# Optimization experiments

Hardware: AMD Instinct MI355X
Metric: run time of the kernel (lower is better)

Reference implementation:

```python
import jax, jax.numpy as jnp
from jax import lax
import numpy as np

DIM = 512
NUM_HEADS = 8
SR = 2


def setup_inputs() -> dict:
    key = jax.random.key(0)
    ks = jax.random.split(key, 7)
    B, H, W = 4, 64, 64
    N = H * W
    C = DIM
    s = 0.02
    return {
        "x": jax.random.normal(ks[0], (B, N, C), dtype=jnp.float32),
        "q_w": jax.random.normal(ks[1], (C, C), dtype=jnp.float32) * s,
        "kv_w": jax.random.normal(ks[2], (2 * C, C), dtype=jnp.float32) * s,
        "sr_w": jax.random.normal(ks[3], (C, C, SR, SR), dtype=jnp.float32) * s,
        "sr_b": jax.random.normal(ks[4], (C,), dtype=jnp.float32) * s,
        "proj_w": jax.random.normal(ks[5], (C, C), dtype=jnp.float32) * s,
        "proj_b": jax.random.normal(ks[6], (C,), dtype=jnp.float32) * s,
        "H": H,
        "W": W,
    }


def reference(x, q_w, kv_w, sr_w, sr_b, proj_w, proj_b, H, W):
    B, N, C = x.shape
    nh = NUM_HEADS
    hd = C // nh
    scale = hd ** -0.5

    # q projection: [B, nh, N, hd]
    q = (x @ q_w.T).reshape(B, N, nh, hd).transpose(0, 2, 1, 3)

    # spatial reduction via strided conv (kernel=stride=SR)
    x_ = x.transpose(0, 2, 1).reshape(B, C, H, W)
    x_ = lax.conv_general_dilated(
        x_, sr_w, window_strides=(SR, SR), padding="VALID",
        dimension_numbers=("NCHW", "OIHW", "NCHW"),
    ) + sr_b[None, :, None, None]
    Nk = (H // SR) * (W // SR)
    x_ = x_.reshape(B, C, Nk).transpose(0, 2, 1)  # [B, Nk, C]

    # kv projection: [2, B, nh, Nk, hd]
    kv = (x_ @ kv_w.T).reshape(B, Nk, 2, nh, hd).transpose(2, 0, 3, 1, 4)
    k, v = kv[0], kv[1]

    attn = jax.nn.softmax(jnp.einsum("bhnd,bhmd->bhnm", q, k) * scale, axis=-1)
    out = jnp.einsum("bhnm,bhmd->bhnd", attn, v)  # [B, nh, N, hd]
    out = out.transpose(0, 2, 1, 3).reshape(B, N, C)
    return out @ proj_w.T + proj_b
```

## Files before the change

### kernel.cpp

```cpp
#include <hip/hip_runtime.h>


typedef __attribute__((ext_vector_type(8)))  short short8;
typedef __attribute__((ext_vector_type(8)))  unsigned short ushort8;
typedef __attribute__((ext_vector_type(4)))  float floatx4;
typedef __attribute__((ext_vector_type(16))) float floatx16;

__device__ inline unsigned short bf16r(float f) {
    union { float f; unsigned u; } v; v.f = f;
    unsigned r = v.u + 0x7fffu + ((v.u >> 16) & 1u);
    return (unsigned short)(r >> 16);
}

__device__ inline unsigned long long pack4ull(float4 v) {
    return (unsigned long long)bf16r(v.x)
         | ((unsigned long long)bf16r(v.y) << 16)
         | ((unsigned long long)bf16r(v.z) << 32)
         | ((unsigned long long)bf16r(v.w) << 48);
}

__device__ inline ushort8 pack8(float4 a, float4 b) {
    ushort8 o;
    o[0] = bf16r(a.x); o[1] = bf16r(a.y); o[2] = bf16r(a.z); o[3] = bf16r(a.w);
    o[4] = bf16r(b.x); o[5] = bf16r(b.y); o[6] = bf16r(b.z); o[7] = bf16r(b.w);
    return o;
}

__device__ inline void gl_lds16(const void* g, void* l) {
    __builtin_amdgcn_global_load_lds(
        (const __attribute__((address_space(1))) unsigned int*)g,
        (__attribute__((address_space(3))) unsigned int*)l, 16, 0, 0);
}

__global__ __launch_bounds__(256)
void prep(const float* __restrict__ x,  const float* __restrict__ qw,
          const float* __restrict__ kvw, const float* __restrict__ srw,
          const float* __restrict__ pw,
          unsigned short* __restrict__ xb,  unsigned short* __restrict__ qwb,
          unsigned short* __restrict__ kvwb, unsigned short* __restrict__ srwb,
          unsigned short* __restrict__ pwb, unsigned short* __restrict__ xrb) {
    const int bid = blockIdx.x;
    if (bid < 2048) {
        const int id = bid * 256 + threadIdx.x;
        const int cq = id & 127, m = id >> 7;
        const int c0 = cq * 4;
        const int b = m >> 10, rem = m & 1023;
        const int oi = rem >> 5, oj = rem & 31;
        const int n00 = oi * 128 + oj * 2;
        const float* bp = x + ((size_t)(b * 4096 + n00)) * 512 + c0;
        const float4 r00 = *(const float4*)bp;
        const float4 r01 = *(const float4*)(bp + 512);
        const float4 r10 = *(const float4*)(bp + 64 * 512);
        const float4 r11 = *(const float4*)(bp + 65 * 512);
        const unsigned long long w00 = pack4ull(r00), w01 = pack4ull(r01),
                                 w10 = pack4ull(r10), w11 = pack4ull(r11);
        unsigned short* xo = xb + ((size_t)(b * 4096 + n00)) * 512 + c0;
        *(unsigned long long*)(xo)            = w00;
        *(unsigned long long*)(xo + 512)      = w01;
        *(unsigned long long*)(xo + 64 * 512) = w10;
        *(unsigned long long*)(xo + 65 * 512) = w11;
        unsigned short* xd = xrb + (size_t)m * 2048 + c0 * 4;
        #pragma unroll
        for (int j = 0; j < 4; ++j) {
            const unsigned long long e =
                  ((w00 >> (16 * j)) & 0xffffull)
                | (((w01 >> (16 * j)) & 0xffffull) << 16)
                | (((w10 >> (16 * j)) & 0xffffull) << 32)
                | (((w11 >> (16 * j)) & 0xffffull) << 48);
            *(unsigned long long*)(xd + j * 4) = e;
        }
    } else {
        const int b2 = bid - 2048;
        const float* src; unsigned short* dst; int off; float sc = 1.f;
        if (b2 < 128)      { src = qw;  dst = qwb;  off = b2 * 256;
                             sc = 0.18033688011112042f;  }
        else if (b2 < 384) { src = kvw; dst = kvwb; off = (b2 - 128) * 256; }
        else if (b2 < 896) { src = srw; dst = srwb; off = (b2 - 384) * 256; }
        else               { src = pw;  dst = pwb;  off = (b2 - 896) * 256; }
        const int idx = off + threadIdx.x;
        float4 a = *(const float4*)(src + (size_t)idx * 8);
        float4 bq = *(const float4*)(src + (size_t)idx * 8 + 4);
        a.x *= sc; a.y *= sc; a.z *= sc; a.w *= sc;
        bq.x *= sc; bq.y *= sc; bq.z *= sc; bq.w *= sc;
        *(ushort8*)(dst + (size_t)idx * 8) = pack8(a, bq);
    }
}

__device__ __forceinline__ void g_stage(
        const unsigned short* __restrict__ A, const unsigned short* __restrict__ B,
        int K, int bm, int bn, int k0, int t,
        unsigned short* AsB, unsigned short* BsB) {
    #pragma unroll
    for (int i = 0; i < 4; ++i) {
        const int c = i * 256 + t;
        const int r = c >> 3, ch = c & 7;
        gl_lds16(A + (size_t)(bm + r) * K + k0 + ((ch ^ (r & 7)) * 8), AsB + c * 8);
    }
    #pragma unroll
    for (int i = 0; i < 2; ++i) {
        const int c = i * 256 + t;
        const int r = c >> 3, ch = c & 7;
        gl_lds16(B + (size_t)(bn + r) * K + k0 + ((ch ^ (r & 7)) * 8), BsB + c * 8);
    }
}

__device__ __forceinline__ void g_comp(
        const unsigned short* AsB, const unsigned short* BsB,
        int lq, int quad, int wrow, floatx4 (&acc)[2][4]) {
    short8 bf[2][4];
    #pragma unroll
    for (int kc = 0; kc < 2; ++kc)
        #pragma unroll
        for (int ni = 0; ni < 4; ++ni) {
            const int r = ni * 16 + lq;
            bf[kc][ni] = *(const short8*)&BsB[r * 64 + (((kc * 4 + quad) ^ (r & 7)) * 8)];
        }
    #pragma unroll
    for (int mi = 0; mi < 2; ++mi) {
        const int r = wrow + mi * 16 + lq;
        #pragma unroll
        for (int kc = 0; kc < 2; ++kc) {
            const short8 af = *(const short8*)&AsB[r * 64 + (((kc * 4 + quad) ^ (r & 7)) * 8)];
            #pragma unroll
            for (int ni = 0; ni < 4; ++ni)
                acc[mi][ni] = __builtin_amdgcn_mfma_f32_16x16x32_bf16(
                    af, bf[kc][ni], acc[mi][ni], 0, 0, 0);
        }
    }
}

__device__ __forceinline__ void g_run(
        const unsigned short* __restrict__ A, const unsigned short* __restrict__ B,
        int K, int bm, int bn, int t, int lq, int quad, int wrow,
        unsigned short (&As)[2][128 * 64], unsigned short (&Bs)[2][64 * 64],
        floatx4 (&acc)[2][4]) {
    g_stage(A, B, K, bm, bn, 0, t, As[0], Bs[0]);
    __syncthreads();
    const int nk = K >> 6;
    for (int ks = 0; ks < nk; ++ks) {
        const int cur = ks & 1;
        if (ks + 1 < nk)
            g_stage(A, B, K, bm, bn, (ks + 1) * 64, t, As[cur ^ 1], Bs[cur ^ 1]);
        __builtin_amdgcn_s_setprio(1);
        g_comp(As[cur], Bs[cur], lq, quad, wrow, acc);
        __builtin_amdgcn_s_setprio(0);
        if (ks + 1 < nk) __syncthreads();
    }
}

__global__ __launch_bounds__(256)
void gemm_qc(const unsigned short* __restrict__ xb, const unsigned short* __restrict__ qwb,
             const unsigned short* __restrict__ xrb, const unsigned short* __restrict__ srwb,
             const float* __restrict__ sr_b,
             unsigned short* __restrict__ qb, unsigned short* __restrict__ xsrb) {
    __shared__ unsigned short As[2][128 * 64];
    __shared__ unsigned short Bs[2][64 * 64];
    const int t = threadIdx.x;
    const int w = t >> 6, l = t & 63;
    const int lq = l & 15, quad = l >> 4;
    const int wrow = w * 32;
    const int bx = blockIdx.x;
    const unsigned short *A, *B; int K, bm; const float* bias; unsigned short* C;
    if (bx < 128) { A = xb;  B = qwb;  K = 512;  bm = bx * 128;         bias = nullptr; C = qb;   }
    else          { A = xrb; B = srwb; K = 2048; bm = (bx - 128) * 128; bias = sr_b;    C = xsrb; }
    const int bn = blockIdx.y * 64;

    floatx4 acc[2][4];
    #pragma unroll
    for (int mi = 0; mi < 2; ++mi)
        #pragma unroll
        for (int ni = 0; ni < 4; ++ni) acc[mi][ni] = (floatx4){0.f, 0.f, 0.f, 0.f};

    g_run(A, B, K, bm, bn, t, lq, quad, wrow, As, Bs, acc);

    #pragma unroll
    for (int ni = 0; ni < 4; ++ni) {
        const int col = bn + ni * 16 + lq;
        const float bv = bias ? bias[col] : 0.f;
        #pragma unroll
        for (int mi = 0; mi < 2; ++mi) {
            const int row0 = bm + wrow + mi * 16 + quad * 4;
            unsigned own[4], mg[4];
            #pragma unroll
            for (int r = 0; r < 4; ++r) own[r] = bf16r(acc[mi][ni][r] + bv);
            #pragma unroll
            for (int r = 0; r < 4; ++r) {
                const unsigned pt = __shfl_xor(own[r], 1);
                mg[r] = (lq & 1) ? (pt | (own[r] << 16)) : (own[r] | (pt << 16));
            }
            const int colb = bn + ni * 16 + (lq & ~1);
            const int rb = (lq & 1) * 2;
            *(unsigned*)(C + (size_t)(row0 + rb)     * 512 + colb) = mg[rb];
            *(unsigned*)(C + (size_t)(row0 + rb + 1) * 512 + colb) = mg[rb + 1];
        }
    }
}

__global__ __launch_bounds__(256)
void gemm_kv(const unsigned short* __restrict__ kvwb, const unsigned short* __restrict__ xsrb,
             unsigned short* __restrict__ Kb, unsigned short* __restrict__ Vt) {
    __shared__ unsigned short As[2][128 * 64];
    __shared__ unsigned short Bs[2][64 * 64];
    const int t = threadIdx.x;
    const int w = t >> 6, l = t & 63;
    const int lq = l & 15, quad = l >> 4;
    const int wrow = w * 32;
    const int id = blockIdx.x;
    const bool isK = id < 256;
    const unsigned short* A = isK ? kvwb : xsrb;
    const unsigned short* B = isK ? xsrb : kvwb + (size_t)512 * 512;
    const int bm = isK ? (id & 3) * 128 : ((id - 256) >> 3) * 128;
    const int bn = isK ? (id >> 2) * 64 : ((id - 256) & 7) * 64;

    floatx4 acc[2][4];
    #pragma unroll
    for (int mi = 0; mi < 2; ++mi)
        #pragma unroll
        for (int ni = 0; ni < 4; ++ni) acc[mi][ni] = (floatx4){0.f, 0.f, 0.f, 0.f};

    g_run(A, B, 512, bm, bn, t, lq, quad, wrow, As, Bs, acc);

    #pragma unroll
    for (int ni = 0; ni < 4; ++ni) {
        const int col = bn + ni * 16 + lq;
        #pragma unroll
        for (int mi = 0; mi < 2; ++mi) {
            const int row0 = bm + wrow + mi * 16 + quad * 4;
            unsigned long long wv = 0;
            #pragma unroll
            for (int r = 0; r < 4; ++r)
                wv |= (unsigned long long)bf16r(acc[mi][ni][r]) << (16 * r);
            if (isK) {
                const int kb = col >> 10, key = col & 1023;
                const int h = row0 >> 6, d0 = row0 & 63;
                *(unsigned long long*)(Kb +
                    (((size_t)(kb * 8 + h)) * 1024 + key) * 64 + d0) = wv;
            } else {
                const int kb = row0 >> 10, key0 = row0 & 1023;
                const int h = col >> 6, d = col & 63;
                *(unsigned long long*)(Vt +
                    (((size_t)(kb * 8 + h)) * 64 + d) * 1024 + key0) = wv;
            }
        }
    }
}

__global__ __launch_bounds__(256)
void gemm_proj(const unsigned short* __restrict__ attb, const unsigned short* __restrict__ pwb,
               const float* __restrict__ pb, float* __restrict__ out) {
    __shared__ unsigned short As[2][128 * 64];
    __shared__ unsigned short Bs[2][64 * 64];
    const int t = threadIdx.x;
    const int w = t >> 6, l = t & 63;
    const int lq = l & 15, quad = l >> 4;
    const int wrow = w * 32;
    const int bm = blockIdx.x * 128, bn = blockIdx.y * 64;

    floatx4 acc[2][4];
    #pragma unroll
    for (int mi = 0; mi < 2; ++mi)
        #pragma unroll
        for (int ni = 0; ni < 4; ++ni) acc[mi][ni] = (floatx4){0.f, 0.f, 0.f, 0.f};

    g_run(attb, pwb, 512, bm, bn, t, lq, quad, wrow, As, Bs, acc);

    #pragma unroll
    for (int ni = 0; ni < 4; ++ni) {
        const int col = bn + ni * 16 + lq;
        const float bv = pb[col];
        #pragma unroll
        for (int mi = 0; mi < 2; ++mi) {
            const int row0 = bm + wrow + mi * 16 + quad * 4;
            #pragma unroll
            for (int r = 0; r < 4; ++r)
                out[(size_t)(row0 + r) * 512 + col] = acc[mi][ni][r] + bv;
        }
    }
}

#define KS2 72

__global__ __launch_bounds__(256)
void attn_mfma32(const unsigned short* __restrict__ qb,
                 const unsigned short* __restrict__ Kb,
                 const unsigned short* __restrict__ Vt,
                 unsigned short* __restrict__ out) {
    __shared__ unsigned short Ks[64 * KS2];
    __shared__ unsigned short Vs[64 * KS2];

    const int t = threadIdx.x;
    const int w = t >> 6;
    const int lane = t & 63;
    const int m32 = lane & 31;
    const int sig = lane >> 5;
    const int n0 = blockIdx.x * 128;
    const int bh = blockIdx.y;
    const int b = bh >> 3, h = bh & 7;

    short8 qf[4];
    {
        const unsigned short* qrow =
            qb + ((size_t)(b * 4096 + n0 + w * 32 + m32)) * 512 + h * 64;
        #pragma unroll
        for (int kc = 0; kc < 4; ++kc)
            qf[kc] = *(const short8*)(qrow + kc * 16 + sig * 8);
    }

    float l_own = 0.f;
    floatx16 O0, O1;
    #pragma unroll
    for (int i = 0; i < 16; ++i) { O0[i] = 0.f; O1[i] = 0.f; }

    const unsigned short* Kg = Kb + (size_t)bh * 1024 * 64;
    const unsigned short* Vg = Vt + (size_t)bh * 64 * 1024;
    const int srow = t >> 2;
    const int sdb  = (t & 3) * 16;

    for (int kt = 0; kt < 16; ++kt) {
        __syncthreads();
        {
            const unsigned short* src = Kg + ((size_t)(kt * 64 + srow)) * 64 + sdb;
            *(ushort8*)&Ks[srow * KS2 + sdb]     = *(const ushort8*)src;
            *(ushort8*)&Ks[srow * KS2 + sdb + 8] = *(const ushort8*)(src + 8);
        }
        {
            const unsigned short* src = Vg + (size_t)srow * 1024 + kt * 64 + sdb;
            *(ushort8*)&Vs[srow * KS2 + sdb]     = *(const ushort8*)src;
            *(ushort8*)&Vs[srow * KS2 + sdb + 8] = *(const ushort8*)(src + 8);
        }
        __syncthreads();

        floatx16 st0, st1;
        #pragma unroll
        for (int i = 0; i < 16; ++i) { st0[i] = 0.f; st1[i] = 0.f; }
        __builtin_amdgcn_s_setprio(1);
        #pragma unroll
        for (int kc = 0; kc < 4; ++kc) {
            const short8 a0 = *(const short8*)&Ks[m32 * KS2 + kc * 16 + sig * 8];
            st0 = __builtin_amdgcn_mfma_f32_32x32x16_bf16(a0, qf[kc], st0, 0, 0, 0);
            const short8 a1 = *(const short8*)&Ks[(32 + m32) * KS2 + kc * 16 + sig * 8];
            st1 = __builtin_amdgcn_mfma_f32_32x32x16_bf16(a1, qf[kc], st1, 0, 0, 0);
        }
        __builtin_amdgcn_s_setprio(0);

        uint2 E[2][4];
        #pragma unroll
        for (int g = 0; g < 2; ++g) {
            #pragma unroll
            for (int qd = 0; qd < 4; ++qd) {
                const float p0 = __builtin_amdgcn_exp2f(g ? st1[qd * 4 + 0] : st0[qd * 4 + 0]);
                const float p1 = __builtin_amdgcn_exp2f(g ? st1[qd * 4 + 1] : st0[qd * 4 + 1]);
                const float p2 = __builtin_amdgcn_exp2f(g ? st1[qd * 4 + 2] : st0[qd * 4 + 2]);
                const float p3 = __builtin_amdgcn_exp2f(g ? st1[qd * 4 + 3] : st0[qd * 4 + 3]);
                E[g][qd].x = __builtin_amdgcn_perm(
                    __float_as_uint(p1), __float_as_uint(p0), 0x07060302u);
                E[g][qd].y = __builtin_amdgcn_perm(
                    __float_as_uint(p3), __float_as_uint(p2), 0x07060302u);
                l_own += (p0 + p1) + (p2 + p3);
            }
        }

        __builtin_amdgcn_s_setprio(1);
        #pragma unroll
        for (int kc = 0; kc < 4; ++kc) {
            const int g = kc >> 1, qlo = (kc & 1) * 2;
            unsigned ax = E[g][qlo].x, bx_ = E[g][qlo + 1].x;
            unsigned ay = E[g][qlo].y, by_ = E[g][qlo + 1].y;
            asm("v_permlane32_swap_b32 %0, %1" : "+v"(ax), "+v"(bx_));
            asm("v_permlane32_swap_b32 %0, %1" : "+v"(ay), "+v"(by_));
            uint4 fr; fr.x = ax; fr.y = ay; fr.z = bx_; fr.w = by_;
            const short8 pa = *(const short8*)&fr;
            const short8 v0 = *(const short8*)&Vs[m32 * KS2 + kc * 16 + sig * 8];
            O0 = __builtin_amdgcn_mfma_f32_32x32x16_bf16(pa, v0, O0, 0, 0, 0);
            const short8 v1 = *(const short8*)&Vs[(32 + m32) * KS2 + kc * 16 + sig * 8];
            O1 = __builtin_amdgcn_mfma_f32_32x32x16_bf16(pa, v1, O1, 0, 0, 0);
        }
        __builtin_amdgcn_s_setprio(0);
    }

    l_own += __shfl_xor(l_own, 32);
    const float inv = 1.0f / l_own;

    float fo0[16], fo1[16];
    #pragma unroll
    for (int r = 0; r < 16; ++r) {
        const float li = __shfl(inv, ((r & 3) + 8 * (r >> 2)) + 4 * sig);
        fo0[r] = O0[r] * li;
        fo1[r] = O1[r] * li;
    }

    #pragma unroll
    for (int gd = 0; gd < 2; ++gd) {
        unsigned mg[16];
        #pragma unroll
        for (int r = 0; r < 16; ++r) {
            const unsigned own = bf16r(gd ? fo1[r] : fo0[r]);
            const unsigned pt = __shfl_xor(own, 1);
            mg[r] = (m32 & 1) ? (pt | (own << 16)) : (own | (pt << 16));
        }
        if ((m32 & 1) == gd) {
            const int colb = h * 64 + gd * 32 + (m32 & ~1);
            #pragma unroll
            for (int r = 0; r < 16; ++r) {
                const int qrow = (r & 3) + 8 * (r >> 2) + 4 * sig;
                const size_t row = (size_t)(b * 4096 + n0 + w * 32 + qrow);
                *(unsigned*)(out + row * 512 + colb) = mg[r];
            }
        }
    }
}

extern "C" void kernel_launch(void* const* d_in, const int* in_sizes, int n_in,
                              void* d_out, int out_size, void* d_ws, size_t ws_size,
                              hipStream_t stream) {
    const float* x      = (const float*)d_in[0];
    const float* q_w    = (const float*)d_in[1];
    const float* kv_w   = (const float*)d_in[2];
    const float* sr_w   = (const float*)d_in[3];
    const float* sr_b   = (const float*)d_in[4];
    const float* proj_w = (const float*)d_in[5];
    const float* proj_b = (const float*)d_in[6];
    float* out = (float*)d_out;

    unsigned short* xb   = (unsigned short*)d_ws;
    unsigned short* attb = xb;
    unsigned short* qb   = xb   + (size_t)16384 * 512;
    unsigned short* xrb  = qb   + (size_t)16384 * 512;
    unsigned short* xsrb = xrb  + (size_t)4096 * 2048;
    unsigned short* qwb  = xsrb + (size_t)4096 * 512;
    unsigned short* kvwb = qwb  + (size_t)512 * 512;
    unsigned short* srwb = kvwb + (size_t)1024 * 512;
    unsigned short* pwb  = srwb + (size_t)512 * 2048;
    unsigned short* Kb   = pwb  + (size_t)512 * 512;
    unsigned short* Vt   = Kb   + (size_t)32 * 1024 * 64;

    const dim3 blk(256);

    prep<<<3072, blk, 0, stream>>>(x, q_w, kv_w, sr_w, proj_w,
                                   xb, qwb, kvwb, srwb, pwb, xrb);

    gemm_qc<<<dim3(160, 8), blk, 0, stream>>>(xb, qwb, xrb, srwb, sr_b, qb, xsrb);

    gemm_kv<<<512, blk, 0, stream>>>(kvwb, xsrb, Kb, Vt);

    attn_mfma32<<<dim3(32, 32), blk, 0, stream>>>(qb, Kb, Vt, attb);

    gemm_proj<<<dim3(128, 8), blk, 0, stream>>>(attb, pwb, proj_b, out);
}
```

Measured before the change: 218.8 us.

## Enlarge GEMM tiles to 128x128 and double attention KV tile with XCD-aware block remap

```diff
diff --git a/kernel.cpp b/kernel.cpp
--- a/kernel.cpp
+++ b/kernel.cpp
@@ -97,7 +97,7 @@
         gl_lds16(A + (size_t)(bm + r) * K + k0 + ((ch ^ (r & 7)) * 8), AsB + c * 8);
     }
     #pragma unroll
-    for (int i = 0; i < 2; ++i) {
+    for (int i = 0; i < 4; ++i) {
         const int c = i * 256 + t;
         const int r = c >> 3, ch = c & 7;
         gl_lds16(B + (size_t)(bn + r) * K + k0 + ((ch ^ (r & 7)) * 8), BsB + c * 8);
@@ -106,34 +106,32 @@
 
 __device__ __forceinline__ void g_comp(
         const unsigned short* AsB, const unsigned short* BsB,
-        int lq, int quad, int wrow, floatx4 (&acc)[2][4]) {
-    short8 bf[2][4];
-    #pragma unroll
-    for (int kc = 0; kc < 2; ++kc)
+        int lq, int quad, int wrow, int wcol, floatx4 (&acc)[4][4]) {
+    #pragma unroll
+    for (int kc = 0; kc < 2; ++kc) {
+        short8 bfq[4];
         #pragma unroll
         for (int ni = 0; ni < 4; ++ni) {
-            const int r = ni * 16 + lq;
-            bf[kc][ni] = *(const short8*)&BsB[r * 64 + (((kc * 4 + quad) ^ (r & 7)) * 8)];
-        }
-    #pragma unroll
-    for (int mi = 0; mi < 2; ++mi) {
-        const int r = wrow + mi * 16 + lq;
-        #pragma unroll
-        for (int kc = 0; kc < 2; ++kc) {
+            const int r = wcol + ni * 16 + lq;
+            bfq[ni] = *(const short8*)&BsB[r * 64 + (((kc * 4 + quad) ^ (r & 7)) * 8)];
+        }
+        #pragma unroll
+        for (int mi = 0; mi < 4; ++mi) {
+            const int r = wrow + mi * 16 + lq;
             const short8 af = *(const short8*)&AsB[r * 64 + (((kc * 4 + quad) ^ (r & 7)) * 8)];
             #pragma unroll
             for (int ni = 0; ni < 4; ++ni)
                 acc[mi][ni] = __builtin_amdgcn_mfma_f32_16x16x32_bf16(
-                    af, bf[kc][ni], acc[mi][ni], 0, 0, 0);
+                    af, bfq[ni], acc[mi][ni], 0, 0, 0);
         }
     }
 }
 
 __device__ __forceinline__ void g_run(
         const unsigned short* __restrict__ A, const unsigned short* __restrict__ B,
-        int K, int bm, int bn, int t, int lq, int quad, int wrow,
-        unsigned short (&As)[2][128 * 64], unsigned short (&Bs)[2][64 * 64],
-        floatx4 (&acc)[2][4]) {
+        int K, int bm, int bn, int t, int lq, int quad, int wrow, int wcol,
+        unsigned short (&As)[2][128 * 64], unsigned short (&Bs)[2][128 * 64],
+        floatx4 (&acc)[4][4]) {
     g_stage(A, B, K, bm, bn, 0, t, As[0], Bs[0]);
     __syncthreads();
     const int nk = K >> 6;
@@ -142,7 +140,7 @@
         if (ks + 1 < nk)
             g_stage(A, B, K, bm, bn, (ks + 1) * 64, t, As[cur ^ 1], Bs[cur ^ 1]);
         __builtin_amdgcn_s_setprio(1);
-        g_comp(As[cur], Bs[cur], lq, quad, wrow, acc);
+        g_comp(As[cur], Bs[cur], lq, quad, wrow, wcol, acc);
         __builtin_amdgcn_s_setprio(0);
         if (ks + 1 < nk) __syncthreads();
     }
@@ -154,31 +152,31 @@
              const float* __restrict__ sr_b,
              unsigned short* __restrict__ qb, unsigned short* __restrict__ xsrb) {
     __shared__ unsigned short As[2][128 * 64];
-    __shared__ unsigned short Bs[2][64 * 64];
+    __shared__ unsigned short Bs[2][128 * 64];
     const int t = threadIdx.x;
     const int w = t >> 6, l = t & 63;
     const int lq = l & 15, quad = l >> 4;
-    const int wrow = w * 32;
+    const int wrow = (w >> 1) * 64, wcol = (w & 1) * 64;
     const int bx = blockIdx.x;
     const unsigned short *A, *B; int K, bm; const float* bias; unsigned short* C;
     if (bx < 128) { A = xb;  B = qwb;  K = 512;  bm = bx * 128;         bias = nullptr; C = qb;   }
     else          { A = xrb; B = srwb; K = 2048; bm = (bx - 128) * 128; bias = sr_b;    C = xsrb; }
-    const int bn = blockIdx.y * 64;
-
-    floatx4 acc[2][4];
-    #pragma unroll
-    for (int mi = 0; mi < 2; ++mi)
+    const int bn = blockIdx.y * 128;
+
+    floatx4 acc[4][4];
+    #pragma unroll
+    for (int mi = 0; mi < 4; ++mi)
         #pragma unroll
         for (int ni = 0; ni < 4; ++ni) acc[mi][ni] = (floatx4){0.f, 0.f, 0.f, 0.f};
 
-    g_run(A, B, K, bm, bn, t, lq, quad, wrow, As, Bs, acc);
+    g_run(A, B, K, bm, bn, t, lq, quad, wrow, wcol, As, Bs, acc);
 
     #pragma unroll
     for (int ni = 0; ni < 4; ++ni) {
-        const int col = bn + ni * 16 + lq;
+        const int col = bn + wcol + ni * 16 + lq;
         const float bv = bias ? bias[col] : 0.f;
         #pragma unroll
-        for (int mi = 0; mi < 2; ++mi) {
+        for (int mi = 0; mi < 4; ++mi) {
             const int row0 = bm + wrow + mi * 16 + quad * 4;
             unsigned own[4], mg[4];
             #pragma unroll
@@ -188,7 +186,7 @@
                 const unsigned pt = __shfl_xor(own[r], 1);
                 mg[r] = (lq & 1) ? (pt | (own[r] << 16)) : (own[r] | (pt << 16));
             }
-            const int colb = bn + ni * 16 + (lq & ~1);
+            const int colb = bn + wcol + ni * 16 + (lq & ~1);
             const int rb = (lq & 1) * 2;
             *(unsigned*)(C + (size_t)(row0 + rb)     * 512 + colb) = mg[rb];
             *(unsigned*)(C + (size_t)(row0 + rb + 1) * 512 + colb) = mg[rb + 1];
@@ -200,31 +198,32 @@
 void gemm_kv(const unsigned short* __restrict__ kvwb, const unsigned short* __restrict__ xsrb,
              unsigned short* __restrict__ Kb, unsigned short* __restrict__ Vt) {
     __shared__ unsigned short As[2][128 * 64];
-    __shared__ unsigned short Bs[2][64 * 64];
+    __shared__ unsigned short Bs[2][128 * 64];
     const int t = threadIdx.x;
     const int w = t >> 6, l = t & 63;
     const int lq = l & 15, quad = l >> 4;
-    const int wrow = w * 32;
+    const int wrow = (w >> 1) * 64, wcol = (w & 1) * 64;
     const int id = blockIdx.x;
-    const bool isK = id < 256;
+    const bool isK = id < 128;
+    const int id2 = isK ? id : id - 128;
     const unsigned short* A = isK ? kvwb : xsrb;
     const unsigned short* B = isK ? xsrb : kvwb + (size_t)512 * 512;
-    const int bm = isK ? (id & 3) * 128 : ((id - 256) >> 3) * 128;
-    const int bn = isK ? (id >> 2) * 64 : ((id - 256) & 7) * 64;
-
-    floatx4 acc[2][4];
-    #pragma unroll
-    for (int mi = 0; mi < 2; ++mi)
+    const int bm = isK ? (id2 & 3) * 128 : (id2 >> 2) * 128;
+    const int bn = isK ? (id2 >> 2) * 128 : (id2 & 3) * 128;
+
+    floatx4 acc[4][4];
+    #pragma unroll
+    for (int mi = 0; mi < 4; ++mi)
         #pragma unroll
         for (int ni = 0; ni < 4; ++ni) acc[mi][ni] = (floatx4){0.f, 0.f, 0.f, 0.f};
 
-    g_run(A, B, 512, bm, bn, t, lq, quad, wrow, As, Bs, acc);
+    g_run(A, B, 512, bm, bn, t, lq, quad, wrow, wcol, As, Bs, acc);
 
     #pragma unroll
     for (int ni = 0; ni < 4; ++ni) {
-        const int col = bn + ni * 16 + lq;
-        #pragma unroll
-        for (int mi = 0; mi < 2; ++mi) {
+        const int col = bn + wcol + ni * 16 + lq;
+        #pragma unroll
+        for (int mi = 0; mi < 4; ++mi) {
             const int row0 = bm + wrow + mi * 16 + quad * 4;
             unsigned long long wv = 0;
             #pragma unroll
@@ -249,27 +248,27 @@
 void gemm_proj(const unsigned short* __restrict__ attb, const unsigned short* __restrict__ pwb,
                const float* __restrict__ pb, float* __restrict__ out) {
     __shared__ unsigned short As[2][128 * 64];
-    __shared__ unsigned short Bs[2][64 * 64];
+    __shared__ unsigned short Bs[2][128 * 64];
     const int t = threadIdx.x;
     const int w = t >> 6, l = t & 63;
     const int lq = l & 15, quad = l >> 4;
-    const int wrow = w * 32;
-    const int bm = blockIdx.x * 128, bn = blockIdx.y * 64;
-
-    floatx4 acc[2][4];
-    #pragma unroll
-    for (int mi = 0; mi < 2; ++mi)
+    const int wrow = (w >> 1) * 64, wcol = (w & 1) * 64;
+    const int bm = blockIdx.x * 128, bn = blockIdx.y * 128;
+
+    floatx4 acc[4][4];
+    #pragma unroll
+    for (int mi = 0; mi < 4; ++mi)
         #pragma unroll
         for (int ni = 0; ni < 4; ++ni) acc[mi][ni] = (floatx4){0.f, 0.f, 0.f, 0.f};
 
-    g_run(attb, pwb, 512, bm, bn, t, lq, quad, wrow, As, Bs, acc);
+    g_run(attb, pwb, 512, bm, bn, t, lq, quad, wrow, wcol, As, Bs, acc);
 
     #pragma unroll
     for (int ni = 0; ni < 4; ++ni) {
-        const int col = bn + ni * 16 + lq;
+        const int col = bn + wcol + ni * 16 + lq;
         const float bv = pb[col];
         #pragma unroll
-        for (int mi = 0; mi < 2; ++mi) {
+        for (int mi = 0; mi < 4; ++mi) {
             const int row0 = bm + wrow + mi * 16 + quad * 4;
             #pragma unroll
             for (int r = 0; r < 4; ++r)
@@ -279,22 +278,25 @@
 }
 
 #define KS2 72
+#define VS2 136
 
 __global__ __launch_bounds__(256)
 void attn_mfma32(const unsigned short* __restrict__ qb,
                  const unsigned short* __restrict__ Kb,
                  const unsigned short* __restrict__ Vt,
                  unsigned short* __restrict__ out) {
-    __shared__ unsigned short Ks[64 * KS2];
-    __shared__ unsigned short Vs[64 * KS2];
+    __shared__ unsigned short Ks[128 * KS2];
+    __shared__ unsigned short Vs[64 * VS2];
 
     const int t = threadIdx.x;
     const int w = t >> 6;
     const int lane = t & 63;
     const int m32 = lane & 31;
     const int sig = lane >> 5;
-    const int n0 = blockIdx.x * 128;
-    const int bh = blockIdx.y;
+    const int hw = blockIdx.x;
+    const int lid = (hw & 7) * 128 + (hw >> 3);
+    const int bh = lid >> 5;
+    const int n0 = (lid & 31) * 128;
     const int b = bh >> 3, h = bh & 7;
 
     short8 qf[4];
@@ -316,66 +318,85 @@
     const int srow = t >> 2;
     const int sdb  = (t & 3) * 16;
 
-    for (int kt = 0; kt < 16; ++kt) {
+    for (int kt2 = 0; kt2 < 8; ++kt2) {
         __syncthreads();
         {
-            const unsigned short* src = Kg + ((size_t)(kt * 64 + srow)) * 64 + sdb;
-            *(ushort8*)&Ks[srow * KS2 + sdb]     = *(const ushort8*)src;
-            *(ushort8*)&Ks[srow * KS2 + sdb + 8] = *(const ushort8*)(src + 8);
+            #pragma unroll
+            for (int i = 0; i < 2; ++i) {
+                const int row = i * 64 + srow;
+                const unsigned short* src =
+                    Kg + ((size_t)(kt2 * 128 + row)) * 64 + sdb;
+                *(ushort8*)&Ks[row * KS2 + sdb]     = *(const ushort8*)src;
+                *(ushort8*)&Ks[row * KS2 + sdb + 8] = *(const ushort8*)(src + 8);
+            }
         }
         {
-            const unsigned short* src = Vg + (size_t)srow * 1024 + kt * 64 + sdb;
-            *(ushort8*)&Vs[srow * KS2 + sdb]     = *(const ushort8*)src;
-            *(ushort8*)&Vs[srow * KS2 + sdb + 8] = *(const ushort8*)(src + 8);
+            #pragma unroll
+            for (int i = 0; i < 2; ++i) {
+                const int colb = i * 64 + sdb;
+                const unsigned short* src =
+                    Vg + (size_t)srow * 1024 + kt2 * 128 + colb;
+                *(ushort8*)&Vs[srow * VS2 + colb]     = *(const ushort8*)src;
+                *(ushort8*)&Vs[srow * VS2 + colb + 8] = *(const ushort8*)(src + 8);
+            }
         }
         __syncthreads();
 
-        floatx16 st0, st1;
-        #pragma unroll
-        for (int i = 0; i < 16; ++i) { st0[i] = 0.f; st1[i] = 0.f; }
-        __builtin_amdgcn_s_setprio(1);
-        #pragma unroll
-        for (int kc = 0; kc < 4; ++kc) {
-            const short8 a0 = *(const short8*)&Ks[m32 * KS2 + kc * 16 + sig * 8];
-            st0 = __builtin_amdgcn_mfma_f32_32x32x16_bf16(a0, qf[kc], st0, 0, 0, 0);
-            const short8 a1 = *(const short8*)&Ks[(32 + m32) * KS2 + kc * 16 + sig * 8];
-            st1 = __builtin_amdgcn_mfma_f32_32x32x16_bf16(a1, qf[kc], st1, 0, 0, 0);
-        }
-        __builtin_amdgcn_s_setprio(0);
-
-        uint2 E[2][4];
-        #pragma unroll
-        for (int g = 0; g < 2; ++g) {
-            #pragma unroll
-            for (int qd = 0; qd < 4; ++qd) {
-                const float p0 = __builtin_amdgcn_exp2f(g ? st1[qd * 4 + 0] : st0[qd * 4 + 0]);
-                const float p1 = __builtin_amdgcn_exp2f(g ? st1[qd * 4 + 1] : st0[qd * 4 + 1]);
-                const float p2 = __builtin_amdgcn_exp2f(g ? st1[qd * 4 + 2] : st0[qd * 4 + 2]);
-                const float p3 = __builtin_amdgcn_exp2f(g ? st1[qd * 4 + 3] : st0[qd * 4 + 3]);
-                E[g][qd].x = __builtin_amdgcn_perm(
-                    __float_as_uint(p1), __float_as_uint(p0), 0x07060302u);
-                E[g][qd].y = __builtin_amdgcn_perm(
-                    __float_as_uint(p3), __float_as_uint(p2), 0x07060302u);
-                l_own += (p0 + p1) + (p2 + p3);
-            }
-        }
-
-        __builtin_amdgcn_s_setprio(1);
-        #pragma unroll
-        for (int kc = 0; kc < 4; ++kc) {
-            const int g = kc >> 1, qlo = (kc & 1) * 2;
-            unsigned ax = E[g][qlo].x, bx_ = E[g][qlo + 1].x;
-            unsigned ay = E[g][qlo].y, by_ = E[g][qlo + 1].y;
-            asm("v_permlane32_swap_b32 %0, %1" : "+v"(ax), "+v"(bx_));
-            asm("v_permlane32_swap_b32 %0, %1" : "+v"(ay), "+v"(by_));
-            uint4 fr; fr.x = ax; fr.y = ay; fr.z = bx_; fr.w = by_;
-            const short8 pa = *(const short8*)&fr;
-            const short8 v0 = *(const short8*)&Vs[m32 * KS2 + kc * 16 + sig * 8];
-            O0 = __builtin_amdgcn_mfma_f32_32x32x16_bf16(pa, v0, O0, 0, 0, 0);
-            const short8 v1 = *(const short8*)&Vs[(32 + m32) * KS2 + kc * 16 + sig * 8];
-            O1 = __builtin_amdgcn_mfma_f32_32x32x16_bf16(pa, v1, O1, 0, 0, 0);
-        }
-        __builtin_amdgcn_s_setprio(0);
+        #pragma unroll
+        for (int half = 0; half < 2; ++half) {
+            const int kof = half * 64;
+
+            floatx16 st0, st1;
+            #pragma unroll
+            for (int i = 0; i < 16; ++i) { st0[i] = 0.f; st1[i] = 0.f; }
+            __builtin_amdgcn_s_setprio(1);
+            #pragma unroll
+            for (int kc = 0; kc < 4; ++kc) {
+                const short8 a0 = *(const short8*)
+                    &Ks[(kof + m32) * KS2 + kc * 16 + sig * 8];
+                st0 = __builtin_amdgcn_mfma_f32_32x32x16_bf16(a0, qf[kc], st0, 0, 0, 0);
+                const short8 a1 = *(const short8*)
+                    &Ks[(kof + 32 + m32) * KS2 + kc * 16 + sig * 8];
+                st1 = __builtin_amdgcn_mfma_f32_32x32x16_bf16(a1, qf[kc], st1, 0, 0, 0);
+            }
+            __builtin_amdgcn_s_setprio(0);
+
+            uint2 E[2][4];
+            #pragma unroll
+            for (int g = 0; g < 2; ++g) {
+                #pragma unroll
+                for (int qd = 0; qd < 4; ++qd) {
+                    const float p0 = __builtin_amdgcn_exp2f(g ? st1[qd * 4 + 0] : st0[qd * 4 + 0]);
+                    const float p1 = __builtin_amdgcn_exp2f(g ? st1[qd * 4 + 1] : st0[qd * 4 + 1]);
+                    const float p2 = __builtin_amdgcn_exp2f(g ? st1[qd * 4 + 2] : st0[qd * 4 + 2]);
+                    const float p3 = __builtin_amdgcn_exp2f(g ? st1[qd * 4 + 3] : st0[qd * 4 + 3]);
+                    E[g][qd].x = __builtin_amdgcn_perm(
+                        __float_as_uint(p1), __float_as_uint(p0), 0x07060302u);
+                    E[g][qd].y = __builtin_amdgcn_perm(
+                        __float_as_uint(p3), __float_as_uint(p2), 0x07060302u);
+                    l_own += (p0 + p1) + (p2 + p3);
+                }
+            }
+
+            __builtin_amdgcn_s_setprio(1);
+            #pragma unroll
+            for (int kc = 0; kc < 4; ++kc) {
+                const int g = kc >> 1, qlo = (kc & 1) * 2;
+                unsigned ax = E[g][qlo].x, bx_ = E[g][qlo + 1].x;
+                unsigned ay = E[g][qlo].y, by_ = E[g][qlo + 1].y;
+                asm("v_permlane32_swap_b32 %0, %1" : "+v"(ax), "+v"(bx_));
+                asm("v_permlane32_swap_b32 %0, %1" : "+v"(ay), "+v"(by_));
+                uint4 fr; fr.x = ax; fr.y = ay; fr.z = bx_; fr.w = by_;
+                const short8 pa = *(const short8*)&fr;
+                const short8 v0 = *(const short8*)
+                    &Vs[m32 * VS2 + kof + kc * 16 + sig * 8];
+                O0 = __builtin_amdgcn_mfma_f32_32x32x16_bf16(pa, v0, O0, 0, 0, 0);
+                const short8 v1 = *(const short8*)
+                    &Vs[(32 + m32) * VS2 + kof + kc * 16 + sig * 8];
+                O1 = __builtin_amdgcn_mfma_f32_32x32x16_bf16(pa, v1, O1, 0, 0, 0);
+            }
+            __builtin_amdgcn_s_setprio(0);
+        }
     }
 
     l_own += __shfl_xor(l_own, 32);
@@ -439,11 +460,11 @@
     prep<<<3072, blk, 0, stream>>>(x, q_w, kv_w, sr_w, proj_w,
                                    xb, qwb, kvwb, srwb, pwb, xrb);
 
-    gemm_qc<<<dim3(160, 8), blk, 0, stream>>>(xb, qwb, xrb, srwb, sr_b, qb, xsrb);
-
-    gemm_kv<<<512, blk, 0, stream>>>(kvwb, xsrb, Kb, Vt);
-
-    attn_mfma32<<<dim3(32, 32), blk, 0, stream>>>(qb, Kb, Vt, attb);
-
-    gemm_proj<<<dim3(128, 8), blk, 0, stream>>>(attb, pwb, proj_b, out);
-}
+    gemm_qc<<<dim3(160, 4), blk, 0, stream>>>(xb, qwb, xrb, srwb, sr_b, qb, xsrb);
+
+    gemm_kv<<<256, blk, 0, stream>>>(kvwb, xsrb, Kb, Vt);
+
+    attn_mfma32<<<1024, blk, 0, stream>>>(qb, Kb, Vt, attb);
+
+    gemm_proj<<<dim3(128, 4), blk, 0, stream>>>(attb, pwb, proj_b, out);
+}
```

Measured after the change: 225.6 us. 1.03x slower.

## Double attention KV tile per barrier, remap blocks, and schedule long GEMM blocks first

Applied to the files above, without the earlier changes.

```diff
diff --git a/kernel.cpp b/kernel.cpp
--- a/kernel.cpp
+++ b/kernel.cpp
@@ -86,7 +86,7 @@
     }
 }
 
-__device__ __forceinline__ void g_stage(
+__device__ __forceinline__ void g_stage64(
         const unsigned short* __restrict__ A, const unsigned short* __restrict__ B,
         int K, int bm, int bn, int k0, int t,
         unsigned short* AsB, unsigned short* BsB) {
@@ -104,7 +104,7 @@
     }
 }
 
-__device__ __forceinline__ void g_comp(
+__device__ __forceinline__ void g_comp64(
         const unsigned short* AsB, const unsigned short* BsB,
         int lq, int quad, int wrow, floatx4 (&acc)[2][4]) {
     short8 bf[2][4];
@@ -129,20 +129,20 @@
     }
 }
 
-__device__ __forceinline__ void g_run(
+__device__ __forceinline__ void g_run64(
         const unsigned short* __restrict__ A, const unsigned short* __restrict__ B,
         int K, int bm, int bn, int t, int lq, int quad, int wrow,
         unsigned short (&As)[2][128 * 64], unsigned short (&Bs)[2][64 * 64],
         floatx4 (&acc)[2][4]) {
-    g_stage(A, B, K, bm, bn, 0, t, As[0], Bs[0]);
+    g_stage64(A, B, K, bm, bn, 0, t, As[0], Bs[0]);
     __syncthreads();
     const int nk = K >> 6;
     for (int ks = 0; ks < nk; ++ks) {
         const int cur = ks & 1;
         if (ks + 1 < nk)
-            g_stage(A, B, K, bm, bn, (ks + 1) * 64, t, As[cur ^ 1], Bs[cur ^ 1]);
+            g_stage64(A, B, K, bm, bn, (ks + 1) * 64, t, As[cur ^ 1], Bs[cur ^ 1]);
         __builtin_amdgcn_s_setprio(1);
-        g_comp(As[cur], Bs[cur], lq, quad, wrow, acc);
+        g_comp64(As[cur], Bs[cur], lq, quad, wrow, acc);
         __builtin_amdgcn_s_setprio(0);
         if (ks + 1 < nk) __syncthreads();
     }
@@ -161,8 +161,8 @@
     const int wrow = w * 32;
     const int bx = blockIdx.x;
     const unsigned short *A, *B; int K, bm; const float* bias; unsigned short* C;
-    if (bx < 128) { A = xb;  B = qwb;  K = 512;  bm = bx * 128;         bias = nullptr; C = qb;   }
-    else          { A = xrb; B = srwb; K = 2048; bm = (bx - 128) * 128; bias = sr_b;    C = xsrb; }
+    if (bx < 32) { A = xrb; B = srwb; K = 2048; bm = bx * 128;        bias = sr_b;    C = xsrb; }
+    else         { A = xb;  B = qwb;  K = 512;  bm = (bx - 32) * 128; bias = nullptr; C = qb;   }
     const int bn = blockIdx.y * 64;
 
     floatx4 acc[2][4];
@@ -171,7 +171,7 @@
         #pragma unroll
         for (int ni = 0; ni < 4; ++ni) acc[mi][ni] = (floatx4){0.f, 0.f, 0.f, 0.f};
 
-    g_run(A, B, K, bm, bn, t, lq, quad, wrow, As, Bs, acc);
+    g_run64(A, B, K, bm, bn, t, lq, quad, wrow, As, Bs, acc);
 
     #pragma unroll
     for (int ni = 0; ni < 4; ++ni) {
@@ -218,7 +218,7 @@
         #pragma unroll
         for (int ni = 0; ni < 4; ++ni) acc[mi][ni] = (floatx4){0.f, 0.f, 0.f, 0.f};
 
-    g_run(A, B, 512, bm, bn, t, lq, quad, wrow, As, Bs, acc);
+    g_run64(A, B, 512, bm, bn, t, lq, quad, wrow, As, Bs, acc);
 
     #pragma unroll
     for (int ni = 0; ni < 4; ++ni) {
@@ -262,7 +262,7 @@
         #pragma unroll
         for (int ni = 0; ni < 4; ++ni) acc[mi][ni] = (floatx4){0.f, 0.f, 0.f, 0.f};
 
-    g_run(attb, pwb, 512, bm, bn, t, lq, quad, wrow, As, Bs, acc);
+    g_run64(attb, pwb, 512, bm, bn, t, lq, quad, wrow, As, Bs, acc);
 
     #pragma unroll
     for (int ni = 0; ni < 4; ++ni) {
@@ -279,22 +279,25 @@
 }
 
 #define KS2 72
+#define VS2 136
 
 __global__ __launch_bounds__(256)
 void attn_mfma32(const unsigned short* __restrict__ qb,
                  const unsigned short* __restrict__ Kb,
                  const unsigned short* __restrict__ Vt,
                  unsigned short* __restrict__ out) {
-    __shared__ unsigned short Ks[64 * KS2];
-    __shared__ unsigned short Vs[64 * KS2];
+    __shared__ unsigned short Ks[128 * KS2];
+    __shared__ unsigned short Vs[64 * VS2];
 
     const int t = threadIdx.x;
     const int w = t >> 6;
     const int lane = t & 63;
     const int m32 = lane & 31;
     const int sig = lane >> 5;
-    const int n0 = blockIdx.x * 128;
-    const int bh = blockIdx.y;
+    const int hw = blockIdx.x;
+    const int lid = (hw & 7) * 128 + (hw >> 3);
+    const int bh = lid >> 5;
+    const int n0 = (lid & 31) * 128;
     const int b = bh >> 3, h = bh & 7;
 
     short8 qf[4];
@@ -316,66 +319,85 @@
     const int srow = t >> 2;
     const int sdb  = (t & 3) * 16;
 
-    for (int kt = 0; kt < 16; ++kt) {
+    for (int kt2 = 0; kt2 < 8; ++kt2) {
         __syncthreads();
         {
-            const unsigned short* src = Kg + ((size_t)(kt * 64 + srow)) * 64 + sdb;
-            *(ushort8*)&Ks[srow * KS2 + sdb]     = *(const ushort8*)src;
-            *(ushort8*)&Ks[srow * KS2 + sdb + 8] = *(const ushort8*)(src + 8);
+            #pragma unroll
+            for (int i = 0; i < 2; ++i) {
+                const int row = i * 64 + srow;
+                const unsigned short* src =
+                    Kg + ((size_t)(kt2 * 128 + row)) * 64 + sdb;
+                *(ushort8*)&Ks[row * KS2 + sdb]     = *(const ushort8*)src;
+                *(ushort8*)&Ks[row * KS2 + sdb + 8] = *(const ushort8*)(src + 8);
+            }
         }
         {
-            const unsigned short* src = Vg + (size_t)srow * 1024 + kt * 64 + sdb;
-            *(ushort8*)&Vs[srow * KS2 + sdb]     = *(const ushort8*)src;
-            *(ushort8*)&Vs[srow * KS2 + sdb + 8] = *(const ushort8*)(src + 8);
+            #pragma unroll
+            for (int i = 0; i < 2; ++i) {
+                const int colb = i * 64 + sdb;
+                const unsigned short* src =
+                    Vg + (size_t)srow * 1024 + kt2 * 128 + colb;
+                *(ushort8*)&Vs[srow * VS2 + colb]     = *(const ushort8*)src;
+                *(ushort8*)&Vs[srow * VS2 + colb + 8] = *(const ushort8*)(src + 8);
+            }
         }
         __syncthreads();
 
-        floatx16 st0, st1;
-        #pragma unroll
-        for (int i = 0; i < 16; ++i) { st0[i] = 0.f; st1[i] = 0.f; }
-        __builtin_amdgcn_s_setprio(1);
-        #pragma unroll
-        for (int kc = 0; kc < 4; ++kc) {
-            const short8 a0 = *(const short8*)&Ks[m32 * KS2 + kc * 16 + sig * 8];
-            st0 = __builtin_amdgcn_mfma_f32_32x32x16_bf16(a0, qf[kc], st0, 0, 0, 0);
-            const short8 a1 = *(const short8*)&Ks[(32 + m32) * KS2 + kc * 16 + sig * 8];
-            st1 = __builtin_amdgcn_mfma_f32_32x32x16_bf16(a1, qf[kc], st1, 0, 0, 0);
-        }
-        __builtin_amdgcn_s_setprio(0);
-
-        uint2 E[2][4];
-        #pragma unroll
-        for (int g = 0; g < 2; ++g) {
-            #pragma unroll
-            for (int qd = 0; qd < 4; ++qd) {
-                const float p0 = __builtin_amdgcn_exp2f(g ? st1[qd * 4 + 0] : st0[qd * 4 + 0]);
-                const float p1 = __builtin_amdgcn_exp2f(g ? st1[qd * 4 + 1] : st0[qd * 4 + 1]);
-                const float p2 = __builtin_amdgcn_exp2f(g ? st1[qd * 4 + 2] : st0[qd * 4 + 2]);
-                const float p3 = __builtin_amdgcn_exp2f(g ? st1[qd * 4 + 3] : st0[qd * 4 + 3]);
-                E[g][qd].x = __builtin_amdgcn_perm(
-                    __float_as_uint(p1), __float_as_uint(p0), 0x07060302u);
-                E[g][qd].y = __builtin_amdgcn_perm(
-                    __float_as_uint(p3), __float_as_uint(p2), 0x07060302u);
-                l_own += (p0 + p1) + (p2 + p3);
-            }
-        }
-
-        __builtin_amdgcn_s_setprio(1);
-        #pragma unroll
-        for (int kc = 0; kc < 4; ++kc) {
-            const int g = kc >> 1, qlo = (kc & 1) * 2;
-            unsigned ax = E[g][qlo].x, bx_ = E[g][qlo + 1].x;
-            unsigned ay = E[g][qlo].y, by_ = E[g][qlo + 1].y;
-            asm("v_permlane32_swap_b32 %0, %1" : "+v"(ax), "+v"(bx_));
-            asm("v_permlane32_swap_b32 %0, %1" : "+v"(ay), "+v"(by_));
-            uint4 fr; fr.x = ax; fr.y = ay; fr.z = bx_; fr.w = by_;
-            const short8 pa = *(const short8*)&fr;
-            const short8 v0 = *(const short8*)&Vs[m32 * KS2 + kc * 16 + sig * 8];
-            O0 = __builtin_amdgcn_mfma_f32_32x32x16_bf16(pa, v0, O0, 0, 0, 0);
-            const short8 v1 = *(const short8*)&Vs[(32 + m32) * KS2 + kc * 16 + sig * 8];
-            O1 = __builtin_amdgcn_mfma_f32_32x32x16_bf16(pa, v1, O1, 0, 0, 0);
-        }
-        __builtin_amdgcn_s_setprio(0);
+        #pragma unroll
+        for (int half = 0; half < 2; ++half) {
+            const int kof = half * 64;
+
+            floatx16 st0, st1;
+            #pragma unroll
+            for (int i = 0; i < 16; ++i) { st0[i] = 0.f; st1[i] = 0.f; }
+            __builtin_amdgcn_s_setprio(1);
+            #pragma unroll
+            for (int kc = 0; kc < 4; ++kc) {
+                const short8 a0 = *(const short8*)
+                    &Ks[(kof + m32) * KS2 + kc * 16 + sig * 8];
+                st0 = __builtin_amdgcn_mfma_f32_32x32x16_bf16(a0, qf[kc], st0, 0, 0, 0);
+                const short8 a1 = *(const short8*)
+                    &Ks[(kof + 32 + m32) * KS2 + kc * 16 + sig * 8];
+                st1 = __builtin_amdgcn_mfma_f32_32x32x16_bf16(a1, qf[kc], st1, 0, 0, 0);
+            }
+            __builtin_amdgcn_s_setprio(0);
+
+            uint2 E[2][4];
+            #pragma unroll
+            for (int g = 0; g < 2; ++g) {
+                #pragma unroll
+                for (int qd = 0; qd < 4; ++qd) {
+                    const float p0 = __builtin_amdgcn_exp2f(g ? st1[qd * 4 + 0] : st0[qd * 4 + 0]);
+                    const float p1 = __builtin_amdgcn_exp2f(g ? st1[qd * 4 + 1] : st0[qd * 4 + 1]);
+                    const float p2 = __builtin_amdgcn_exp2f(g ? st1[qd * 4 + 2] : st0[qd * 4 + 2]);
+                    const float p3 = __builtin_amdgcn_exp2f(g ? st1[qd * 4 + 3] : st0[qd * 4 + 3]);
+                    E[g][qd].x = __builtin_amdgcn_perm(
+                        __float_as_uint(p1), __float_as_uint(p0), 0x07060302u);
+                    E[g][qd].y = __builtin_amdgcn_perm(
+                        __float_as_uint(p3), __float_as_uint(p2), 0x07060302u);
+                    l_own += (p0 + p1) + (p2 + p3);
+                }
+            }
+
+            __builtin_amdgcn_s_setprio(1);
+            #pragma unroll
+            for (int kc = 0; kc < 4; ++kc) {
+                const int g = kc >> 1, qlo = (kc & 1) * 2;
+                unsigned ax = E[g][qlo].x, bx_ = E[g][qlo + 1].x;
+                unsigned ay = E[g][qlo].y, by_ = E[g][qlo + 1].y;
+                asm("v_permlane32_swap_b32 %0, %1" : "+v"(ax), "+v"(bx_));
+                asm("v_permlane32_swap_b32 %0, %1" : "+v"(ay), "+v"(by_));
+                uint4 fr; fr.x = ax; fr.y = ay; fr.z = bx_; fr.w = by_;
+                const short8 pa = *(const short8*)&fr;
+                const short8 v0 = *(const short8*)
+                    &Vs[m32 * VS2 + kof + kc * 16 + sig * 8];
+                O0 = __builtin_amdgcn_mfma_f32_32x32x16_bf16(pa, v0, O0, 0, 0, 0);
+                const short8 v1 = *(const short8*)
+                    &Vs[(32 + m32) * VS2 + kof + kc * 16 + sig * 8];
+                O1 = __builtin_amdgcn_mfma_f32_32x32x16_bf16(pa, v1, O1, 0, 0, 0);
+            }
+            __builtin_amdgcn_s_setprio(0);
+        }
     }
 
     l_own += __shfl_xor(l_own, 32);
@@ -443,7 +465,7 @@
 
     gemm_kv<<<512, blk, 0, stream>>>(kvwb, xsrb, Kb, Vt);
 
-    attn_mfma32<<<dim3(32, 32), blk, 0, stream>>>(qb, Kb, Vt, attb);
+    attn_mfma32<<<1024, blk, 0, stream>>>(qb, Kb, Vt, attb);
 
     gemm_proj<<<dim3(128, 8), blk, 0, stream>>>(attb, pwb, proj_b, out);
 }
```

Result: no change. 216.9 us (-0.9%).
